# Kernel tuning notes

Measured on AMD Instinct MI355X. Metric: run time of the kernel, lower is better.

## Reference

```python
import jax, jax.numpy as jnp
import numpy as np
import math

EMB = 1024
HEADS = 16
VOCAB = 32000


def gelu_tanh(x):
    c = math.sqrt(2.0 / math.pi)
    return 0.5 * x * (1.0 + jnp.tanh(c * (x + 0.044715 * x * x * x)))


def layernorm(x, w, b, eps=1e-5):
    mean = jnp.mean(x, axis=-1, keepdims=True)
    var = jnp.var(x, axis=-1, keepdims=True)  # unbiased=False
    return w * ((x - mean) / jnp.sqrt(var + eps)) + b


def setup_inputs() -> dict:
    key = jax.random.key(0)
    ks = jax.random.split(key, 12)
    E, H, V = EMB, HEADS, VOCAB
    s = 1.0 / math.sqrt(E)
    return {
        "x": jax.random.normal(ks[0], (2, 2048, E), dtype=jnp.float32),
        "W_q": jax.random.normal(ks[1], (E, E), dtype=jnp.float32) * s,
        "W_k": jax.random.normal(ks[2], (E, E), dtype=jnp.float32) * s,
        "W_v": jax.random.normal(ks[3], (E, E), dtype=jnp.float32) * s,
        "ln1_w": jnp.ones((E,), jnp.float32),
        "ln1_b": jnp.zeros((E,), jnp.float32),
        "ln2_w": jnp.ones((E,), jnp.float32),
        "ln2_b": jnp.zeros((E,), jnp.float32),
        "ff_w1": jax.random.normal(ks[4], (E, 4 * E), dtype=jnp.float32) * s,
        "ff_b1": jnp.zeros((4 * E,), jnp.float32),
        "ff_w2": jax.random.normal(ks[5], (4 * E, E), dtype=jnp.float32) * (0.5 * s),
        "ff_b2": jnp.zeros((E,), jnp.float32),
        "proj_w": jax.random.normal(ks[6], (E, V), dtype=jnp.float32) * s,
        "proj_b": jnp.zeros((V,), jnp.float32),
    }


def attention(x, W_q, W_k, W_v):
    B, S, E = x.shape
    H = HEADS
    D = E // H
    q = (x @ W_q).reshape(B, S, H, D).transpose(0, 2, 1, 3)  # [B,H,S,D]
    k = (x @ W_k).reshape(B, S, H, D).transpose(0, 2, 1, 3)
    v = (x @ W_v).reshape(B, S, H, D).transpose(0, 2, 1, 3)
    scores = jnp.einsum("bhqd,bhkd->bhqk", q, k) / math.sqrt(D)
    causal = jnp.tril(jnp.ones((S, S), dtype=bool))
    scores = jnp.where(causal[None, None], scores, -jnp.inf)
    w = jax.nn.softmax(scores, axis=-1)
    ctx = jnp.einsum("bhqk,bhkd->bhqd", w, v)
    return ctx.transpose(0, 2, 1, 3).reshape(B, S, E)


def reference(x, W_q, W_k, W_v, ln1_w, ln1_b, ln2_w, ln2_b,
              ff_w1, ff_b1, ff_w2, ff_b2, proj_w, proj_b):
    # pre-LN attention block (dropout = identity, drop_rate=0)
    h = x + attention(layernorm(x, ln1_w, ln1_b), W_q, W_k, W_v)
    # pre-LN FFN block
    ff_in = layernorm(h, ln2_w, ln2_b)
    ff = gelu_tanh(ff_in @ ff_w1 + ff_b1) @ ff_w2 + ff_b2
    h = h + ff
    return h @ proj_w + proj_b
```

## Files before the change

### kernel.cpp

```cpp
#include <hip/hip_runtime.h>

using u16 = unsigned short;
typedef __attribute__((ext_vector_type(8))) short bf16x8;
typedef __attribute__((ext_vector_type(4))) float f32x4;

#define DEVI __device__ __forceinline__

DEVI float bf2f(u16 u){ union{ unsigned v; float f; } x; x.v = ((unsigned)u)<<16; return x.f; }
DEVI u16 f2bf(float f){ union{ float f; unsigned v; } x; x.f = f;
  unsigned r = x.v + 0x7FFFu + ((x.v>>16)&1u); return (u16)(r>>16); }

DEVI float gelu_f(float x){
  float y = 0.7978845608028654f*(x + 0.044715f*x*x*x);
  y = fminf(fmaxf(y, -30.f), 30.f);
  float e = __expf(2.f*y);
  return 0.5f*x*(1.f + (e-1.f)/(e+1.f));
}

DEVI void gload_lds16(const void* g, void* l){
  __builtin_amdgcn_global_load_lds((const __attribute__((address_space(1))) void*)g,
                                   (__attribute__((address_space(3))) void*)l, 16, 0, 0);
}

#define BARM asm volatile("s_barrier" ::: "memory")
#define LGKM0 asm volatile("s_waitcnt lgkmcnt(0)" ::: "memory")
#define VM8  asm volatile("s_waitcnt vmcnt(8)"  ::: "memory")
#define VM0  asm volatile("s_waitcnt vmcnt(0)"  ::: "memory")

__global__ __launch_bounds__(256) void wconv_kernel(const float* __restrict__ in,
                                                    u16* __restrict__ out, int R, int C){
  __shared__ u16 t[32][33];
  int c0 = blockIdx.x*32, r0 = blockIdx.y*32;
  int tc = threadIdx.x & 31, tr = threadIdx.x >> 5;
  #pragma unroll
  for (int i=0;i<4;i++){
    int r = tr + i*8;
    t[r][tc] = f2bf(in[(size_t)(r0+r)*C + (c0+tc)]);
  }
  __syncthreads();
  #pragma unroll
  for (int i=0;i<4;i++){
    int r = tr + i*8;
    out[(size_t)(c0+r)*R + (r0+tc)] = t[tc][r];
  }
}

DEVI void block_reduce2(float& s1, float& s2, int tid){
  #pragma unroll
  for (int off=1; off<64; off<<=1){ s1 += __shfl_xor(s1, off); s2 += __shfl_xor(s2, off); }
  __shared__ float red[8];
  int wid = tid>>6;
  if ((tid&63)==0){ red[wid*2]=s1; red[wid*2+1]=s2; }
  __syncthreads();
  s1 = red[0]+red[2]+red[4]+red[6];
  s2 = red[1]+red[3]+red[5]+red[7];
}

__global__ __launch_bounds__(256) void ln_kernel(const float* __restrict__ x,
    const float* __restrict__ w, const float* __restrict__ b, u16* __restrict__ out){
  int row = blockIdx.x, tid = threadIdx.x;
  float4 v = ((const float4*)(x + (size_t)row*1024))[tid];
  float s1 = v.x+v.y+v.z+v.w;
  float s2 = v.x*v.x+v.y*v.y+v.z*v.z+v.w*v.w;
  block_reduce2(s1,s2,tid);
  float mean = s1*(1.f/1024.f);
  float var  = s2*(1.f/1024.f) - mean*mean;
  float inv  = rsqrtf(var + 1e-5f);
  float4 wv = ((const float4*)w)[tid];
  float4 bv = ((const float4*)b)[tid];
  ushort4 o;
  o.x = f2bf(wv.x*((v.x-mean)*inv)+bv.x);
  o.y = f2bf(wv.y*((v.y-mean)*inv)+bv.y);
  o.z = f2bf(wv.z*((v.z-mean)*inv)+bv.z);
  o.w = f2bf(wv.w*((v.w-mean)*inv)+bv.w);
  ((ushort4*)(out + (size_t)row*1024))[tid] = o;
}

__global__ __launch_bounds__(256) void resln_kernel(const float* __restrict__ x,
    const u16* __restrict__ ctx, const float* __restrict__ w, const float* __restrict__ b,
    float* __restrict__ h, u16* __restrict__ hb){
  int row = blockIdx.x, tid = threadIdx.x;
  float4 xv = ((const float4*)(x + (size_t)row*1024))[tid];
  ushort4 cv = ((const ushort4*)(ctx + (size_t)row*1024))[tid];
  float4 hv;
  hv.x = xv.x + bf2f(cv.x); hv.y = xv.y + bf2f(cv.y);
  hv.z = xv.z + bf2f(cv.z); hv.w = xv.w + bf2f(cv.w);
  ((float4*)(h + (size_t)row*1024))[tid] = hv;
  float s1 = hv.x+hv.y+hv.z+hv.w;
  float s2 = hv.x*hv.x+hv.y*hv.y+hv.z*hv.z+hv.w*hv.w;
  block_reduce2(s1,s2,tid);
  float mean = s1*(1.f/1024.f);
  float var  = s2*(1.f/1024.f) - mean*mean;
  float inv  = rsqrtf(var + 1e-5f);
  float4 wv = ((const float4*)w)[tid];
  float4 bv = ((const float4*)b)[tid];
  ushort4 o;
  o.x = f2bf(wv.x*((hv.x-mean)*inv)+bv.x);
  o.y = f2bf(wv.y*((hv.y-mean)*inv)+bv.y);
  o.z = f2bf(wv.z*((hv.z-mean)*inv)+bv.z);
  o.w = f2bf(wv.w*((hv.w-mean)*inv)+bv.w);
  ((ushort4*)(hb + (size_t)row*1024))[tid] = o;
}

template<class EpiF>
DEVI void gemm8_core(const u16* __restrict__ A, const u16* __restrict__ Bt,
                     int K, int m0, int n0, EpiF epi){
  __shared__ __align__(16) u16 As[2][16384];
  __shared__ __align__(16) u16 Bs[2][16384];
  const int tid = threadIdx.x;
  const int wid = tid>>6, lane = tid&63;
  const int wr = wid>>2, wc = wid&3;
  const int g = lane>>4, l16 = lane&15;
  const int wq = wid&3;
  const int lr = lane>>3, ls = lane&7;

  f32x4 acc[8][4] = {};

  const u16* aSrc[2][2]; unsigned aDst[2][2];
  #pragma unroll
  for (int qm=0;qm<2;qm++)
    #pragma unroll
    for (int j=0;j<2;j++){
      int r = wr*128 + qm*64 + wq*16 + j*8 + lr;
      aSrc[qm][j] = A + (size_t)(m0 + r)*K + ((ls ^ (r&7))*8);
      aDst[qm][j] = (unsigned)(((wr*128 + qm*64)*8 + (wq*2+j)*64)*16);
    }
  const u16* bSrc[2][2]; unsigned bDst[2][2];
  #pragma unroll
  for (int qn=0;qn<2;qn++)
    #pragma unroll
    for (int j=0;j<2;j++){
      int r = wc*64 + qn*32 + wr*16 + j*8 + lr;
      bSrc[qn][j] = Bt + (size_t)(n0 + r)*K + ((ls ^ (r&7))*8);
      bDst[qn][j] = (unsigned)(((wc*64 + qn*32)*8 + (wr*2+j)*64)*16);
    }

  auto stageAll = [&](int buf, int kc){
    char* ab = (char*)&As[buf][0];
    char* bb = (char*)&Bs[buf][0];
    #pragma unroll
    for (int j=0;j<2;j++) gload_lds16(aSrc[0][j] + kc, ab + aDst[0][j]);
    #pragma unroll
    for (int j=0;j<2;j++) gload_lds16(bSrc[0][j] + kc, bb + bDst[0][j]);
    #pragma unroll
    for (int j=0;j<2;j++) gload_lds16(bSrc[1][j] + kc, bb + bDst[1][j]);
    #pragma unroll
    for (int j=0;j<2;j++) gload_lds16(aSrc[1][j] + kc, ab + aDst[1][j]);
  };
  auto ldA = [&](int buf, int qm, bf16x8 (&a)[4][2]){
    const char* base = (const char*)&As[buf][0];
    #pragma unroll
    for (int i=0;i<4;i++){
      int r = wr*128 + qm*64 + i*16 + l16;
      #pragma unroll
      for (int kk=0;kk<2;kk++)
        a[i][kk] = *(const bf16x8*)(base + r*128 + ((kk*64 + g*16) ^ ((l16&7)<<4)));
    }
  };
  auto ldB = [&](int buf, int qn, bf16x8 (&b)[2][2]){
    const char* base = (const char*)&Bs[buf][0];
    #pragma unroll
    for (int i=0;i<2;i++){
      int r = wc*64 + qn*32 + i*16 + l16;
      #pragma unroll
      for (int kk=0;kk<2;kk++)
        b[i][kk] = *(const bf16x8*)(base + r*128 + ((kk*64 + g*16) ^ ((l16&7)<<4)));
    }
  };
  auto mm = [&](int qm, int qn, bf16x8 (&a)[4][2], bf16x8 (&b)[2][2]){
    __builtin_amdgcn_s_setprio(1);
    #pragma unroll
    for (int i=0;i<4;i++)
      #pragma unroll
      for (int n=0;n<2;n++)
        #pragma unroll
        for (int kk=0;kk<2;kk++)
          acc[qm*4+i][qn*2+n] =
            __builtin_amdgcn_mfma_f32_16x16x32_bf16(a[i][kk], b[n][kk], acc[qm*4+i][qn*2+n], 0,0,0);
    __builtin_amdgcn_s_setprio(0);
  };

  const int NT = K>>6;
  stageAll(0, 0);
  stageAll(1, 64);

  bf16x8 a[4][2], b0[2][2], b1[2][2];
  int cur = 0;
  for (int t=0; t<NT; ++t){
    if (t < NT-1) { VM8; } else { VM0; }
    BARM;
    ldA(cur,0,a); ldB(cur,0,b0); ldB(cur,1,b1);
    mm(0,0,a,b0);
    mm(0,1,a,b1);
    ldA(cur,1,a);
    LGKM0; BARM;
    if (t+2 < NT) stageAll(cur, (t+2)<<6);
    mm(1,0,a,b0);
    mm(1,1,a,b1);
    cur ^= 1;
  }
  BARM;
  epi((char*)&As[0][0], (char*)&Bs[0][0], acc);
}

template<class EpiF>
DEVI void gemm128_core(const u16* __restrict__ A, const u16* __restrict__ Bt,
                       int Kstride, int Klen, int m0, int n0, EpiF epi){
  __shared__ __align__(16) u16 As[2][8192];
  __shared__ __align__(16) u16 Bs[2][8192];
  const int tid = threadIdx.x;
  const int wid = tid>>6, lane = tid&63;
  const int wr = wid>>1, wc = wid&1;
  const int g = lane>>4, l16 = lane&15;
  const int lr = lane>>3, ls = lane&7;

  f32x4 acc[4][4] = {};

  const u16* aSrc[4]; unsigned aDst[4];
  const u16* bSrc[4];
  #pragma unroll
  for (int j=0;j<4;j++){
    int r = wid*32 + j*8 + lr;
    aSrc[j] = A  + (size_t)(m0 + r)*Kstride + ((ls ^ lr)*8);
    bSrc[j] = Bt + (size_t)(n0 + r)*Kstride + ((ls ^ lr)*8);
    aDst[j] = (unsigned)((wid*32 + j*8)*128);
  }

  auto stageAll = [&](int buf, int kc){
    char* ab = (char*)&As[buf][0];
    char* bb = (char*)&Bs[buf][0];
    #pragma unroll
    for (int j=0;j<4;j++) gload_lds16(aSrc[j] + kc, ab + aDst[j]);
    #pragma unroll
    for (int j=0;j<4;j++) gload_lds16(bSrc[j] + kc, bb + aDst[j]);
  };
  auto ldA = [&](int buf, bf16x8 (&a)[4][2]){
    const char* base = (const char*)&As[buf][0];
    #pragma unroll
    for (int i=0;i<4;i++){
      int r = wr*64 + i*16 + l16;
      #pragma unroll
      for (int kk=0;kk<2;kk++)
        a[i][kk] = *(const bf16x8*)(base + r*128 + ((kk*64 + g*16) ^ ((l16&7)<<4)));
    }
  };
  auto ldB = [&](int buf, bf16x8 (&b)[4][2]){
    const char* base = (const char*)&Bs[buf][0];
    #pragma unroll
    for (int i=0;i<4;i++){
      int r = wc*64 + i*16 + l16;
      #pragma unroll
      for (int kk=0;kk<2;kk++)
        b[i][kk] = *(const bf16x8*)(base + r*128 + ((kk*64 + g*16) ^ ((l16&7)<<4)));
    }
  };

  const int NT = Klen>>6;
  stageAll(0, 0);
  stageAll(1, 64);

  bf16x8 a[4][2], b[4][2];
  int cur = 0;
  for (int t=0; t<NT; ++t){
    if (t < NT-1) { VM8; } else { VM0; }
    BARM;
    ldA(cur, a); ldB(cur, b);
    __builtin_amdgcn_s_setprio(1);
    #pragma unroll
    for (int i=0;i<2;i++)
      #pragma unroll
      for (int n=0;n<4;n++)
        #pragma unroll
        for (int kk=0;kk<2;kk++)
          acc[i][n] = __builtin_amdgcn_mfma_f32_16x16x32_bf16(a[i][kk], b[n][kk], acc[i][n], 0,0,0);
    __builtin_amdgcn_s_setprio(0);
    LGKM0; BARM;
    if (t+2 < NT) stageAll(cur, (t+2)<<6);
    __builtin_amdgcn_s_setprio(1);
    #pragma unroll
    for (int i=2;i<4;i++)
      #pragma unroll
      for (int n=0;n<4;n++)
        #pragma unroll
        for (int kk=0;kk<2;kk++)
          acc[i][n] = __builtin_amdgcn_mfma_f32_16x16x32_bf16(a[i][kk], b[n][kk], acc[i][n], 0,0,0);
    __builtin_amdgcn_s_setprio(0);
    cur ^= 1;
  }
  BARM;
  epi(acc);
}

DEVI int xcd_swz(int id, int nwg){ return (id&7)*(nwg>>3) + (id>>3); }

__global__ __launch_bounds__(512,2) void proj8_kernel(const u16* __restrict__ hfb,
    const u16* __restrict__ pwt, const float* __restrict__ pb, float* __restrict__ out){
  const int xcd = blockIdx.x & 7, c = blockIdx.x >> 3;
  const int mt = 2*xcd + (c & 1);
  const int nt = c >> 1;
  const int m0 = mt*256, n0 = nt*256;
  gemm8_core(hfb, pwt, 1024, m0, n0,
    [&](char* sA, char* sB, f32x4 (&acc)[8][4]){
      const int tid = threadIdx.x;
      const int wid = tid>>6, lane = tid&63;
      const int wr = wid>>2, wc = wid&3;
      const int g = lane>>4, l16 = lane&15;
      float* ep = (float*)((wid<4 ? sA : sB) + (wid&3)*16384);
      float bb[4];
      #pragma unroll
      for (int nf=0;nf<4;nf++) bb[nf] = pb[n0 + wc*64 + nf*16 + l16];
      #pragma unroll
      for (int p=0;p<2;p++){
        #pragma unroll
        for (int mf4=0;mf4<4;mf4++){
          int mf = p*4 + mf4;
          #pragma unroll
          for (int nf=0;nf<4;nf++){
            #pragma unroll
            for (int r=0;r<4;r++)
              ep[(mf4*16 + g*4 + r)*64 + nf*16 + l16] = acc[mf][nf][r] + bb[nf];
          }
        }
        LGKM0;
        #pragma unroll
        for (int it=0;it<16;it++){
          int rl = it*4 + g;
          f32x4 v = *(const f32x4*)&ep[rl*64 + l16*4];
          int grow = m0 + wr*128 + p*64 + rl;
          __builtin_nontemporal_store(v,
            (f32x4*)&out[(size_t)grow*32000 + n0 + wc*64 + l16*4]);
        }
        LGKM0;
      }
    });
}

__global__ __launch_bounds__(512,2) void ffn1_8_kernel(const u16* __restrict__ hb,
    const u16* __restrict__ w1t, const float* __restrict__ b1, u16* __restrict__ gout){
  int swz = xcd_swz(blockIdx.x, gridDim.x);
  int mt = swz & 15, nt = swz >> 4;
  const int m0 = mt*256, n0 = nt*256;
  gemm8_core(hb, w1t, 1024, m0, n0,
    [&](char*, char*, f32x4 (&acc)[8][4]){
      const int tid = threadIdx.x;
      const int wid = tid>>6, lane = tid&63;
      const int wr = wid>>2, wc = wid&3;
      const int g = lane>>4, l16 = lane&15;
      #pragma unroll
      for (int mf=0;mf<8;mf++)
        #pragma unroll
        for (int nf=0;nf<4;nf++){
          int row = m0 + wr*128 + mf*16 + g*4;
          int col = n0 + wc*64 + nf*16 + l16;
          float bb = b1[col];
          #pragma unroll
          for (int r=0;r<4;r++)
            gout[(size_t)(row+r)*4096 + col] = f2bf(gelu_f(acc[mf][nf][r] + bb));
        }
    });
}

__global__ __launch_bounds__(512,2) void qkv8_kernel(const u16* __restrict__ xn,
    const u16* __restrict__ wqt, const u16* __restrict__ wkt, const u16* __restrict__ wvt,
    u16* __restrict__ qo, u16* __restrict__ ko, u16* __restrict__ vo){
  int swz = xcd_swz(blockIdx.x, gridDim.x);
  int mt = swz & 15, ntt = swz >> 4;
  int sel = ntt >> 2;
  const u16* Bt = (sel==0)?wqt:((sel==1)?wkt:wvt);
  u16* outp = (sel==0)?qo:((sel==1)?ko:vo);
  const int m0 = mt*256, n0 = (ntt&3)*256;
  gemm8_core(xn, Bt, 1024, m0, n0,
    [&](char*, char*, f32x4 (&acc)[8][4]){
      const int tid = threadIdx.x;
      const int wid = tid>>6, lane = tid&63;
      const int wr = wid>>2, wc = wid&3;
      const int g = lane>>4, l16 = lane&15;
      #pragma unroll
      for (int mf=0;mf<8;mf++)
        #pragma unroll
        for (int nf=0;nf<4;nf++){
          int row = m0 + wr*128 + mf*16 + g*4;
          int col = n0 + wc*64 + nf*16 + l16;
          #pragma unroll
          for (int r=0;r<4;r++)
            outp[(size_t)(row+r)*1024 + col] = f2bf(acc[mf][nf][r]);
        }
    });
}

__global__ __launch_bounds__(256,2) void ffn2_part_kernel(const u16* __restrict__ gin,
    const u16* __restrict__ w2t, float* __restrict__ p0, float* __restrict__ p1){
  const int xcd = blockIdx.x & 7, c = blockIdx.x >> 3;
  const int ks = c & 1;
  const int cc = c >> 1;
  const int mt = 4*xcd + (cc & 3);
  const int nt = cc >> 2;
  const int m0 = mt*128, n0 = nt*128;
  float* part = ks ? p1 : p0;
  gemm128_core(gin + ks*2048, w2t + ks*2048, 4096, 2048, m0, n0,
    [&](f32x4 (&acc)[4][4]){
      const int tid = threadIdx.x;
      const int wid = tid>>6, lane = tid&63;
      const int wr = wid>>1, wc = wid&1;
      const int g = lane>>4, l16 = lane&15;
      #pragma unroll
      for (int i=0;i<4;i++)
        #pragma unroll
        for (int nf=0;nf<4;nf++){
          int row = m0 + wr*64 + i*16 + g*4;
          int col = n0 + wc*64 + nf*16 + l16;
          #pragma unroll
          for (int r=0;r<4;r++)
            part[(size_t)(row+r)*1024 + col] = acc[i][nf][r];
        }
    });
}

__global__ __launch_bounds__(256) void ffn2_comb_kernel(const float* __restrict__ p0,
    const float* __restrict__ p1, const float* __restrict__ b2,
    const float* __restrict__ h, u16* __restrict__ hfb){
  int row = blockIdx.x, tid = threadIdx.x;
  float4 a = ((const float4*)(p0 + (size_t)row*1024))[tid];
  float4 b = ((const float4*)(p1 + (size_t)row*1024))[tid];
  float4 hv = ((const float4*)(h + (size_t)row*1024))[tid];
  float4 bv = ((const float4*)b2)[tid];
  ushort4 o;
  o.x = f2bf(hv.x + a.x + b.x + bv.x);
  o.y = f2bf(hv.y + a.y + b.y + bv.y);
  o.z = f2bf(hv.z + a.z + b.z + bv.z);
  o.w = f2bf(hv.w + a.w + b.w + bv.w);
  ((ushort4*)(hfb + (size_t)row*1024))[tid] = o;
}

__global__ __launch_bounds__(256) void attn_kernel(const u16* __restrict__ q,
    const u16* __restrict__ k, const u16* __restrict__ v, u16* __restrict__ ctx){
  __shared__ u16 Qs[64*64];
  __shared__ u16 Ks[2][64*64], Vt[2][64*64];
  __shared__ u16 Ps[4][16*64];
  const int tid = threadIdx.x, lane = tid&63, wid = tid>>6;
  const int g = lane>>4, l16 = lane&15;
  const int b = blockIdx.x>>4, hh = blockIdx.x&15;
  const int qb = 31 - blockIdx.y;
  const size_t tokbase = (size_t)b*2048;
  const int hoff = hh*64;

  #pragma unroll
  for (int j=0;j<2;j++){
    int c = j*256 + tid;
    int r = c>>3, c8 = c&7;
    uint4 val = *(const uint4*)(q + (tokbase + qb*64 + r)*1024 + hoff + c8*8);
    *(uint4*)((char*)Qs + r*128 + ((c8*16) ^ ((r&7)<<4))) = val;
  }
  uint4 kreg[2], vreg[2];
  #pragma unroll
  for (int j=0;j<2;j++){
    int c = j*256 + tid;
    int r = c>>3, c8 = c&7;
    kreg[j] = *(const uint4*)(k + (tokbase + r)*1024 + hoff + c8*8);
    vreg[j] = *(const uint4*)(v + (tokbase + r)*1024 + hoff + c8*8);
  }
  #pragma unroll
  for (int j=0;j<2;j++){
    int c = j*256 + tid;
    int r = c>>3, c8 = c&7;
    *(uint4*)((char*)&Ks[0][0] + r*128 + ((c8*16) ^ ((r&7)<<4))) = kreg[j];
    union{ uint4 u; u16 s[8]; } uu; uu.u = vreg[j];
    #pragma unroll
    for (int e=0;e<8;e++){
      int d = c8*8 + e;
      *(u16*)((char*)&Vt[0][0] + d*128 + ((r*2) ^ ((d&7)<<4))) = uu.s[e];
    }
  }
  __syncthreads();

  bf16x8 qa[2];
  const int qrow_l = wid*16 + l16;
  #pragma unroll
  for (int kk=0;kk<2;kk++)
    qa[kk] = *(const bf16x8*)((const char*)Qs + qrow_l*128 + ((kk*64 + g*16) ^ ((qrow_l&7)<<4)));

  float m_r[4], l_r[4];
  f32x4 o_acc[4] = {};
  #pragma unroll
  for (int r=0;r<4;r++){ m_r[r] = -1e30f; l_r[r] = 0.f; }

  for (int kt=0; kt<=qb; kt++){
    const int cur = kt&1, nxt = cur^1;
    if (kt < qb){
      const int kv0n = (kt+1)*64;
      #pragma unroll
      for (int j=0;j<2;j++){
        int c = j*256 + tid;
        int r = c>>3, c8 = c&7;
        kreg[j] = *(const uint4*)(k + (tokbase + kv0n + r)*1024 + hoff + c8*8);
        vreg[j] = *(const uint4*)(v + (tokbase + kv0n + r)*1024 + hoff + c8*8);
      }
    }
    const int kv0 = kt*64;
    f32x4 s[4] = {};
    #pragma unroll
    for (int c=0;c<4;c++){
      #pragma unroll
      for (int kk=0;kk<2;kk++){
        int krow = c*16 + l16;
        bf16x8 kb = *(const bf16x8*)((const char*)&Ks[cur][0] + krow*128 + ((kk*64 + g*16) ^ ((krow&7)<<4)));
        s[c] = __builtin_amdgcn_mfma_f32_16x16x32_bf16(qa[kk], kb, s[c], 0,0,0);
      }
    }
    const int qrow0 = qb*64 + wid*16 + g*4;
    float sv[4][4];
    #pragma unroll
    for (int c=0;c<4;c++){
      #pragma unroll
      for (int r=0;r<4;r++){
        float xx = s[c][r] * 0.125f;
        if (kt==qb){
          int kvabs = kv0 + c*16 + l16;
          if (kvabs > qrow0 + r) xx = -1e30f;
        }
        sv[c][r] = xx;
      }
    }
    #pragma unroll
    for (int r=0;r<4;r++){
      float rm = fmaxf(fmaxf(sv[0][r],sv[1][r]),fmaxf(sv[2][r],sv[3][r]));
      #pragma unroll
      for (int off=1; off<16; off<<=1) rm = fmaxf(rm, __shfl_xor(rm, off));
      float mn  = fmaxf(m_r[r], rm);
      float fac = __expf(m_r[r] - mn);
      float rs = 0.f;
      const int prow = g*4 + r;
      #pragma unroll
      for (int c=0;c<4;c++){
        float p = __expf(sv[c][r] - mn);
        rs += p;
        *(u16*)((char*)&Ps[wid][0] + prow*128 + (((c*16+l16)*2) ^ ((prow&7)<<4))) = f2bf(p);
      }
      #pragma unroll
      for (int off=1; off<16; off<<=1) rs += __shfl_xor(rs, off);
      m_r[r] = mn;
      l_r[r] = l_r[r]*fac + rs;
      #pragma unroll
      for (int c=0;c<4;c++) o_acc[c][r] *= fac;
    }
    bf16x8 pa[2];
    #pragma unroll
    for (int kk=0;kk<2;kk++)
      pa[kk] = *(const bf16x8*)((const char*)&Ps[wid][0] + l16*128 + ((kk*64 + g*16) ^ ((l16&7)<<4)));
    #pragma unroll
    for (int c=0;c<4;c++){
      #pragma unroll
      for (int kk=0;kk<2;kk++){
        int vrow = c*16 + l16;
        bf16x8 vb = *(const bf16x8*)((const char*)&Vt[cur][0] + vrow*128 + ((kk*64 + g*16) ^ ((vrow&7)<<4)));
        o_acc[c] = __builtin_amdgcn_mfma_f32_16x16x32_bf16(pa[kk], vb, o_acc[c], 0,0,0);
      }
    }
    if (kt < qb){
      #pragma unroll
      for (int j=0;j<2;j++){
        int c = j*256 + tid;
        int r = c>>3, c8 = c&7;
        *(uint4*)((char*)&Ks[nxt][0] + r*128 + ((c8*16) ^ ((r&7)<<4))) = kreg[j];
        union{ uint4 u; u16 s[8]; } uu; uu.u = vreg[j];
        #pragma unroll
        for (int e=0;e<8;e++){
          int d = c8*8 + e;
          *(u16*)((char*)&Vt[nxt][0] + d*128 + ((r*2) ^ ((d&7)<<4))) = uu.s[e];
        }
      }
    }
    __syncthreads();
  }
  #pragma unroll
  for (int c=0;c<4;c++){
    #pragma unroll
    for (int r=0;r<4;r++){
      float o = o_acc[c][r] / l_r[r];
      size_t tok = tokbase + qb*64 + wid*16 + g*4 + r;
      ctx[tok*1024 + hoff + c*16 + l16] = f2bf(o);
    }
  }
}

extern "C" void kernel_launch(void* const* d_in, const int* in_sizes, int n_in,
                              void* d_out, int out_size, void* d_ws, size_t ws_size,
                              hipStream_t stream){
  (void)in_sizes; (void)n_in; (void)out_size; (void)ws_size;
  const float* x    = (const float*)d_in[0];
  const float* Wq   = (const float*)d_in[1];
  const float* Wk   = (const float*)d_in[2];
  const float* Wv   = (const float*)d_in[3];
  const float* ln1w = (const float*)d_in[4];
  const float* ln1b = (const float*)d_in[5];
  const float* ln2w = (const float*)d_in[6];
  const float* ln2b = (const float*)d_in[7];
  const float* fw1  = (const float*)d_in[8];
  const float* fb1  = (const float*)d_in[9];
  const float* fw2  = (const float*)d_in[10];
  const float* fb2  = (const float*)d_in[11];
  const float* pw   = (const float*)d_in[12];
  const float* pb   = (const float*)d_in[13];

  char* ob = (char*)d_out;
  u16* wqt = (u16*)(ob + 0);
  u16* wkt = (u16*)(ob + 2097152);
  u16* wvt = (u16*)(ob + 4194304);
  u16* w1t = (u16*)(ob + 6291456);
  u16* w2t = (u16*)(ob + 14680064);
  u16* xn  = (u16*)(ob + 23068672);
  u16* qbf = (u16*)(ob + 31457280);
  u16* kbf = (u16*)(ob + 39845888);
  u16* vbf = (u16*)(ob + 48234496);
  u16* ctx = (u16*)(ob + 56623104);
  float* h = (float*)(ob + 65011712);
  u16* hb  = (u16*)(ob + 81788928);
  u16* gbuf= (u16*)(ob + 90177536);
  float* p0= (float*)(ob + 134217728);
  float* p1= (float*)(ob + 150994944);

  char* wsb = (char*)d_ws;
  u16* pwt = (u16*)(wsb + 0);
  u16* hfb = (u16*)(wsb + 65536000);

  wconv_kernel<<<dim3(32,32)  ,256,0,stream>>>(Wq , wqt, 1024, 1024);
  wconv_kernel<<<dim3(32,32)  ,256,0,stream>>>(Wk , wkt, 1024, 1024);
  wconv_kernel<<<dim3(32,32)  ,256,0,stream>>>(Wv , wvt, 1024, 1024);
  wconv_kernel<<<dim3(128,32) ,256,0,stream>>>(fw1, w1t, 1024, 4096);
  wconv_kernel<<<dim3(32,128) ,256,0,stream>>>(fw2, w2t, 4096, 1024);
  wconv_kernel<<<dim3(1000,32),256,0,stream>>>(pw , pwt, 1024, 32000);

  ln_kernel      <<<4096,256,0,stream>>>(x, ln1w, ln1b, xn);
  qkv8_kernel    <<<192,512,0,stream>>>(xn, wqt, wkt, wvt, qbf, kbf, vbf);
  attn_kernel    <<<dim3(32,32),256,0,stream>>>(qbf, kbf, vbf, ctx);
  resln_kernel   <<<4096,256,0,stream>>>(x, ctx, ln2w, ln2b, h, hb);
  ffn1_8_kernel  <<<256,512,0,stream>>>(hb, w1t, fb1, gbuf);
  ffn2_part_kernel<<<512,256,0,stream>>>(gbuf, w2t, p0, p1);
  ffn2_comb_kernel<<<4096,256,0,stream>>>(p0, p1, fb2, h, hfb);
  proj8_kernel   <<<2000,512,0,stream>>>(hfb, pwt, pb, (float*)d_out);
}
```

Before: 601.0 us.

## Interleave split global-to-LDS staging with MFMA quadrants in the 256-tile GEMM loop

Splits the monolithic per-iteration prefetch into per-quadrant A and B staging calls. These are placed between the four MFMA quadrant blocks, each fenced by barriers and LDS waits. The aim is to spread global-to-LDS traffic across the compute phase, so memory issue overlaps MFMA work instead of arriving in one burst. The cost is several extra workgroup barriers per K-step, which may add synchronisation stalls.

Result: slower. 642.9 us (+7.0%).

```diff
diff --git a/kernel.cpp b/kernel.cpp
--- a/kernel.cpp
+++ b/kernel.cpp
@@ -135,17 +135,15 @@
       bDst[qn][j] = (unsigned)(((wc*64 + qn*32)*8 + (wr*2+j)*64)*16);
     }
 
-  auto stageAll = [&](int buf, int kc){
-    char* ab = (char*)&As[buf][0];
-    char* bb = (char*)&Bs[buf][0];
-    #pragma unroll
-    for (int j=0;j<2;j++) gload_lds16(aSrc[0][j] + kc, ab + aDst[0][j]);
-    #pragma unroll
-    for (int j=0;j<2;j++) gload_lds16(bSrc[0][j] + kc, bb + bDst[0][j]);
-    #pragma unroll
-    for (int j=0;j<2;j++) gload_lds16(bSrc[1][j] + kc, bb + bDst[1][j]);
-    #pragma unroll
-    for (int j=0;j<2;j++) gload_lds16(aSrc[1][j] + kc, ab + aDst[1][j]);
+  auto stA = [&](int buf, int qm, int kc){
+    char* base = (char*)&As[buf][0];
+    #pragma unroll
+    for (int j=0;j<2;j++) gload_lds16(aSrc[qm][j] + kc, base + aDst[qm][j]);
+  };
+  auto stB = [&](int buf, int qn, int kc){
+    char* base = (char*)&Bs[buf][0];
+    #pragma unroll
+    for (int j=0;j<2;j++) gload_lds16(bSrc[qn][j] + kc, base + bDst[qn][j]);
   };
   auto ldA = [&](int buf, int qm, bf16x8 (&a)[4][2]){
     const char* base = (const char*)&As[buf][0];
@@ -181,25 +179,29 @@
   };
 
   const int NT = K>>6;
-  stageAll(0, 0);
-  stageAll(1, 64);
+  stA(0,0,0);  stB(0,0,0);  stA(0,1,0);  stB(0,1,0);
+  stA(1,0,64); stB(1,0,64); stA(1,1,64); stB(1,1,64);
+  VM8; BARM;
 
   bf16x8 a[4][2], b0[2][2], b1[2][2];
-  int cur = 0;
   for (int t=0; t<NT; ++t){
-    if (t < NT-1) { VM8; } else { VM0; }
+    const int cur = t&1;
+    const int k2 = (t+2)<<6;
+    const bool st = (t+2) < NT;
+    ldA(cur,0,a); ldB(cur,0,b0);
+    BARM; LGKM0; mm(0,0,a,b0); BARM;
+    ldB(cur,1,b1);
+    if (st) stA(cur,0,k2);
+    BARM; LGKM0; mm(0,1,a,b1); BARM;
+    ldA(cur,1,a);
+    if (st) stB(cur,0,k2);
+    BARM; LGKM0; mm(1,0,a,b0); BARM;
+    if (st) { stB(cur,1,k2); stA(cur,1,k2); }
+    BARM; mm(1,1,a,b1);
+    if (st) { VM8; } else { VM0; }
     BARM;
-    ldA(cur,0,a); ldB(cur,0,b0); ldB(cur,1,b1);
-    mm(0,0,a,b0);
-    mm(0,1,a,b1);
-    ldA(cur,1,a);
-    LGKM0; BARM;
-    if (t+2 < NT) stageAll(cur, (t+2)<<6);
-    mm(1,0,a,b0);
-    mm(1,1,a,b1);
-    cur ^= 1;
-  }
-  BARM;
+  }
+  LGKM0; BARM;
   epi((char*)&As[0][0], (char*)&Bs[0][0], acc);
 }
 
```
